# Optimization experiments

Measured on AMD Instinct MI355X. Metric: run time of the kernel, lower is better.

Reference implementation:

```python
import jax, jax.numpy as jnp
import numpy as np
from jax import lax

B, D, K = 65536, 256, 32  # batch, num_latent_dims, flow_depth


def setup_inputs() -> dict:
    key = jax.random.key(0)
    k1, k2, k3, k4, k5 = jax.random.split(key, 5)
    X = jax.random.normal(k1, (B, D), dtype=jnp.float32)
    h = jax.random.normal(k2, (B, D), dtype=jnp.float32)  # passed through, unused by planar math
    u = jax.random.normal(k3, (K, D), dtype=jnp.float32) * 0.1
    w = jax.random.normal(k4, (K, D), dtype=jnp.float32) * 0.1
    b = jax.random.normal(k5, (K,), dtype=jnp.float32) * 0.1
    return {"X": X, "h": h, "u": u, "w": w, "b": b}


def _planar_chain(z0, u, w, b):
    """Sequential planar normalizing flow: z_{k+1} = z_k + u_hat_k * tanh(w_k.z_k + b_k)."""

    def step(z, params):
        u_k, w_k, b_k = params  # (D,), (D,), scalar
        # enforce invertibility: u_hat so that w.u_hat >= -1
        wu = jnp.dot(w_k, u_k)
        u_hat = u_k + (jax.nn.softplus(wu) - 1.0 - wu) * w_k / jnp.dot(w_k, w_k)
        lin = z @ w_k + b_k              # (B,)
        t = jnp.tanh(lin)                # (B,)
        z_new = z + t[:, None] * u_hat[None, :]
        # psi = (1 - t^2) w ; log|det J| = log|1 + psi.u_hat|
        log_det = jnp.log(jnp.abs(1.0 + (1.0 - t * t) * jnp.dot(w_k, u_hat)) + 1e-8)
        return z_new, log_det

    z_final, log_dets = lax.scan(step, z0, (u, w, b))
    return z_final, log_dets  # (B, D), (K, B)


def reference(X, h, u, w, b):
    z = X.reshape(X.shape[0], X.shape[1])  # view(B, D, -1) then view(B, D) -> (B, D)
    z_final, log_det_jacobians = _planar_chain(z, u, w, b)
    return z_final, log_det_jacobians
```

## Files before the change

### kernel.cpp

```cpp
#include <hip/hip_runtime.h>


#define B_ 65536
#define D_ 256
#define ROWS 128
#define GRID (B_ / ROWS)

#define WS_WT 0
#define WS_UH 8192
#define WS_G  16384
#define WS_C  17408

#define SW(c) (4 * (((c) + ((c) >> 3)) & 7))

__global__ __launch_bounds__(256) void nf_gen(const float* __restrict__ u_in,
                                              const float* __restrict__ w_in,
                                              float* __restrict__ ws) {
  __shared__ float wTg[8192];
  __shared__ float ug[8192];
  __shared__ float wu_s[32], ww_s[32], coefs_s[32];
  const int t = threadIdx.x;
  {
    const int k = t & 31, d0 = (t >> 5) * 32;
    const float4* wp = (const float4*)(w_in + k * 256 + d0);
#pragma unroll
    for (int q = 0; q < 8; ++q) {
      float4 v = wp[q];
      wTg[(d0 + q * 4 + 0) * 32 + k] = v.x;
      wTg[(d0 + q * 4 + 1) * 32 + k] = v.y;
      wTg[(d0 + q * 4 + 2) * 32 + k] = v.z;
      wTg[(d0 + q * 4 + 3) * 32 + k] = v.w;
    }
#pragma unroll
    for (int q = 0; q < 8; ++q)
      ((float4*)ug)[t + 256 * q] = ((const float4*)u_in)[t + 256 * q];
  }
  __syncthreads();
  const int k = t & 31, jg = t >> 5;
  float m1[4] = {0.f, 0.f, 0.f, 0.f}, m2[4] = {0.f, 0.f, 0.f, 0.f};
#pragma unroll 4
  for (int dc = 0; dc < 64; ++dc) {
    float wk[4];
    float4 wj[4], uj[4];
#pragma unroll
    for (int i = 0; i < 4; ++i) wk[i] = wTg[(dc * 4 + i) * 32 + k];
#pragma unroll
    for (int i = 0; i < 4; ++i) wj[i] = *(const float4*)&wTg[(dc * 4 + i) * 32 + jg * 4];
#pragma unroll
    for (int i = 0; i < 4; ++i) uj[i] = *(const float4*)&ug[(jg * 4 + i) * 256 + dc * 4];
#pragma unroll
    for (int i = 0; i < 4; ++i) {
      m1[i] = fmaf(uj[i].x, wk[0], m1[i]);
      m1[i] = fmaf(uj[i].y, wk[1], m1[i]);
      m1[i] = fmaf(uj[i].z, wk[2], m1[i]);
      m1[i] = fmaf(uj[i].w, wk[3], m1[i]);
    }
    const float* w0 = (const float*)&wj[0];
    const float* w1 = (const float*)&wj[1];
    const float* w2 = (const float*)&wj[2];
    const float* w3 = (const float*)&wj[3];
#pragma unroll
    for (int i = 0; i < 4; ++i) {
      m2[i] = fmaf(w0[i], wk[0], m2[i]);
      m2[i] = fmaf(w1[i], wk[1], m2[i]);
      m2[i] = fmaf(w2[i], wk[2], m2[i]);
      m2[i] = fmaf(w3[i], wk[3], m2[i]);
    }
  }
  if ((k >> 2) == jg) {
    wu_s[k] = m1[k & 3];
    ww_s[k] = m2[k & 3];
  }
  __syncthreads();
  if (t < 32) {
    float wu = wu_s[t], ww = ww_s[t];
    float sp = fmaxf(wu, 0.f) + log1pf(__expf(-fabsf(wu)));
    coefs_s[t] = (sp - 1.f - wu) / ww;
    ws[WS_C + t] = sp - 1.f;
  }
  __syncthreads();
#pragma unroll
  for (int i = 0; i < 4; ++i)
    ws[WS_G + k * 32 + jg * 4 + i] = fmaf(coefs_s[jg * 4 + i], m2[i], m1[i]);
  {
    const int k2 = t >> 3, d0 = (t & 7) * 32;
    const float ck = coefs_s[k2];
    const float4* up = (const float4*)(u_in + k2 * 256 + d0);
    const float4* wp2 = (const float4*)(w_in + k2 * 256 + d0);
    float4* od = (float4*)(ws + WS_UH + k2 * 256 + d0);
#pragma unroll
    for (int q = 0; q < 8; ++q) {
      float4 uv = up[q], wv = wp2[q];
      uv.x = fmaf(ck, wv.x, uv.x);
      uv.y = fmaf(ck, wv.y, uv.y);
      uv.z = fmaf(ck, wv.z, uv.z);
      uv.w = fmaf(ck, wv.w, uv.w);
      od[q] = uv;
    }
  }
#pragma unroll
  for (int q = 0; q < 8; ++q)
    ((float4*)(ws + WS_WT))[t + 256 * q] = ((const float4*)wTg)[t + 256 * q];
}

__global__ __launch_bounds__(256) void nf_fused(const float* __restrict__ X,
                                                const float* __restrict__ b_in,
                                                const float* __restrict__ ws,
                                                float* __restrict__ out) {
  __shared__ float wT[8192];
  __shared__ float us[8192];
  __shared__ float Xs[4096];
  const int t = threadIdx.x;
  const int row0 = blockIdx.x * ROWS;
  const int xoff = (t >> 6) * 32 + ((t >> 3) & 7) * 4;
  const int kq4 = (t & 7) * 4;
  const int row_ld = t >> 3;
  const int cl = t & 7;

#pragma unroll
  for (int q = 0; q < 8; ++q)
    ((float4*)wT)[t + 256 * q] = ((const float4*)(ws + WS_WT))[t + 256 * q];
#pragma unroll
  for (int q = 0; q < 8; ++q)
    ((float4*)us)[t + 256 * q] = ((const float4*)(ws + WS_UH))[t + 256 * q];

  float4 pf[4];
  auto load_stage = [&](int s) {
#pragma unroll
    for (int p = 0; p < 4; ++p)
      pf[p] = *(const float4*)(X + (size_t)(row0 + p * 32 + row_ld) * 256 + s * 32 + cl * 4);
  };
  auto store_stage = [&]() {
#pragma unroll
    for (int p = 0; p < 4; ++p) {
      const float f[4] = {pf[p].x, pf[p].y, pf[p].z, pf[p].w};
#pragma unroll
      for (int i = 0; i < 4; ++i) {
        const int c = cl * 4 + i;
        Xs[c * 128 + ((p * 32 + row_ld + SW(c)) & 127)] = f[i];
      }
    }
  };

  load_stage(0);
  __syncthreads();

  float p[4][4];
#pragma unroll
  for (int a = 0; a < 4; ++a)
#pragma unroll
    for (int b = 0; b < 4; ++b) p[a][b] = 0.f;

  for (int s = 0; s < 8; ++s) {
    store_stage();
    __syncthreads();
    if (s < 7) load_stage(s + 1);
#pragma unroll 8
    for (int dl = 0; dl < 32; ++dl) {
      float4 xv = *(const float4*)&Xs[dl * 128 + ((xoff + SW(dl)) & 127)];
      float4 wv = *(const float4*)&wT[(s * 32 + dl) * 32 + kq4];
      const float xr[4] = {xv.x, xv.y, xv.z, xv.w};
      const float wk[4] = {wv.x, wv.y, wv.z, wv.w};
#pragma unroll
      for (int a = 0; a < 4; ++a)
#pragma unroll
        for (int b = 0; b < 4; ++b) p[a][b] = fmaf(xr[a], wk[b], p[a][b]);
    }
    __syncthreads();
  }

#pragma unroll
  for (int b = 0; b < 4; ++b)
    *(float4*)&wT[(kq4 + b) * 128 + xoff] = make_float4(p[0][b], p[1][b], p[2][b], p[3][b]);
#pragma unroll
  for (int i = 0; i < 4; ++i) {
    const int e = t * 4 + i;
    Xs[(e >> 5) * 33 + (e & 31)] = ws[WS_G + e];
  }
  if (t < 32) {
    Xs[1536 + t] = ws[WS_C + t];
    Xs[1568 + t] = b_in[t];
  }
  __syncthreads();

  if (t < 128) {
    float pfull[32];
#pragma unroll
    for (int j = 0; j < 32; ++j) pfull[j] = wT[j * 128 + t] + Xs[1568 + j];
    float tvv[32];
#pragma unroll
    for (int kk = 0; kk < 32; ++kk) {
      float la = pfull[kk], lb = 0.f;
      const float* gp = &Xs[kk * 33];
#pragma unroll
      for (int j = 0; j + 1 < kk; j += 2) {
        la = fmaf(tvv[j], gp[j], la);
        lb = fmaf(tvv[j + 1], gp[j + 1], lb);
      }
      if (kk & 1) la = fmaf(tvv[kk - 1], gp[kk - 1], la);
      float lin = la + lb;
      float e = __expf(2.f * lin);
      float tk = 1.f - 2.f / (e + 1.f);
      tvv[kk] = tk;
      wT[4096 + kk * 128 + t] = tk;
      float val = fabsf(fmaf(1.f - tk * tk, Xs[1536 + kk], 1.f)) + 1e-8f;
      out[(size_t)B_ * D_ + (size_t)kk * B_ + row0 + t] = __logf(val);
    }
  }
  __syncthreads();

  const int cq8 = (t & 7) * 8;
  for (int cb = 0; cb < 4; ++cb) {
    const int c0 = cb * 64 + cq8;
    float acc[4][8];
#pragma unroll
    for (int a = 0; a < 4; ++a) {
      const float4 x0 = *(const float4*)(X + (size_t)(row0 + xoff + a) * 256 + c0);
      const float4 x1 = *(const float4*)(X + (size_t)(row0 + xoff + a) * 256 + c0 + 4);
      acc[a][0] = x0.x; acc[a][1] = x0.y; acc[a][2] = x0.z; acc[a][3] = x0.w;
      acc[a][4] = x1.x; acc[a][5] = x1.y; acc[a][6] = x1.z; acc[a][7] = x1.w;
    }
#pragma unroll 8
    for (int kk = 0; kk < 32; ++kk) {
      float4 t4 = *(const float4*)&wT[4096 + kk * 128 + xoff];
      float4 u0 = *(const float4*)&us[kk * 256 + c0];
      float4 u1 = *(const float4*)&us[kk * 256 + c0 + 4];
      const float tr[4] = {t4.x, t4.y, t4.z, t4.w};
      const float uk[8] = {u0.x, u0.y, u0.z, u0.w, u1.x, u1.y, u1.z, u1.w};
#pragma unroll
      for (int a = 0; a < 4; ++a)
#pragma unroll
        for (int b = 0; b < 8; ++b) acc[a][b] = fmaf(tr[a], uk[b], acc[a][b]);
    }
#pragma unroll
    for (int a = 0; a < 4; ++a) {
      float4* op = (float4*)(out + (size_t)(row0 + xoff + a) * 256 + c0);
      op[0] = make_float4(acc[a][0], acc[a][1], acc[a][2], acc[a][3]);
      op[1] = make_float4(acc[a][4], acc[a][5], acc[a][6], acc[a][7]);
    }
  }
}

extern "C" void kernel_launch(void* const* d_in, const int* in_sizes, int n_in,
                              void* d_out, int out_size, void* d_ws, size_t ws_size,
                              hipStream_t stream) {
  const float* X = (const float*)d_in[0];
  const float* u = (const float*)d_in[2];
  const float* w = (const float*)d_in[3];
  const float* b = (const float*)d_in[4];
  float* out = (float*)d_out;
  float* ws = (float*)d_ws;

  nf_gen<<<1, 256, 0, stream>>>(u, w, ws);
  nf_fused<<<GRID, 256, 0, stream>>>(X, b, ws, out);
}
```

Baseline: 204.5 us.

## Drop LDS staging of X, w and u_hat; read them directly from global memory

```diff
diff --git a/kernel.cpp b/kernel.cpp
--- a/kernel.cpp
+++ b/kernel.cpp
@@ -11,7 +11,12 @@
 #define WS_G  16384
 #define WS_C  17408
 
-#define SW(c) (4 * (((c) + ((c) >> 3)) & 7))
+#define P_STR 132
+#define T_OFF 4224
+#define G_OFF 8448
+#define C_OFF 9504
+#define BB_OFF 9536
+#define LDS_FLOATS 9568
 
 __global__ __launch_bounds__(256) void nf_gen(const float* __restrict__ u_in,
                                               const float* __restrict__ w_in,
@@ -107,91 +112,68 @@
                                                 const float* __restrict__ b_in,
                                                 const float* __restrict__ ws,
                                                 float* __restrict__ out) {
-  __shared__ float wT[8192];
-  __shared__ float us[8192];
-  __shared__ float Xs[4096];
+  __shared__ float lds[LDS_FLOATS];
+
   const int t = threadIdx.x;
   const int row0 = blockIdx.x * ROWS;
   const int xoff = (t >> 6) * 32 + ((t >> 3) & 7) * 4;
   const int kq4 = (t & 7) * 4;
-  const int row_ld = t >> 3;
-  const int cl = t & 7;
-
-#pragma unroll
-  for (int q = 0; q < 8; ++q)
-    ((float4*)wT)[t + 256 * q] = ((const float4*)(ws + WS_WT))[t + 256 * q];
-#pragma unroll
-  for (int q = 0; q < 8; ++q)
-    ((float4*)us)[t + 256 * q] = ((const float4*)(ws + WS_UH))[t + 256 * q];
-
-  float4 pf[4];
-  auto load_stage = [&](int s) {
-#pragma unroll
-    for (int p = 0; p < 4; ++p)
-      pf[p] = *(const float4*)(X + (size_t)(row0 + p * 32 + row_ld) * 256 + s * 32 + cl * 4);
-  };
-  auto store_stage = [&]() {
-#pragma unroll
-    for (int p = 0; p < 4; ++p) {
-      const float f[4] = {pf[p].x, pf[p].y, pf[p].z, pf[p].w};
-#pragma unroll
-      for (int i = 0; i < 4; ++i) {
-        const int c = cl * 4 + i;
-        Xs[c * 128 + ((p * 32 + row_ld + SW(c)) & 127)] = f[i];
+  const int cq8 = (t & 7) * 8;
+
+  float p[4][4];
+#pragma unroll
+  for (int a = 0; a < 4; ++a)
+#pragma unroll
+    for (int b2 = 0; b2 < 4; ++b2) p[a][b2] = 0.f;
+  {
+    const float* wbase = ws + WS_WT + kq4;
+    const float* xb = X + (size_t)(row0 + xoff) * 256;
+#pragma unroll 2
+    for (int dq = 0; dq < 64; ++dq) {
+      float4 wr[4];
+#pragma unroll
+      for (int i = 0; i < 4; ++i) wr[i] = *(const float4*)(wbase + (dq * 4 + i) * 32);
+      float4 xr[4];
+#pragma unroll
+      for (int a = 0; a < 4; ++a) xr[a] = *(const float4*)(xb + a * 256 + dq * 4);
+#pragma unroll
+      for (int a = 0; a < 4; ++a) {
+        const float xf[4] = {xr[a].x, xr[a].y, xr[a].z, xr[a].w};
+#pragma unroll
+        for (int i = 0; i < 4; ++i) {
+          p[a][0] = fmaf(xf[i], wr[i].x, p[a][0]);
+          p[a][1] = fmaf(xf[i], wr[i].y, p[a][1]);
+          p[a][2] = fmaf(xf[i], wr[i].z, p[a][2]);
+          p[a][3] = fmaf(xf[i], wr[i].w, p[a][3]);
+        }
       }
     }
-  };
-
-  load_stage(0);
-  __syncthreads();
-
-  float p[4][4];
-#pragma unroll
-  for (int a = 0; a < 4; ++a)
-#pragma unroll
-    for (int b = 0; b < 4; ++b) p[a][b] = 0.f;
-
-  for (int s = 0; s < 8; ++s) {
-    store_stage();
-    __syncthreads();
-    if (s < 7) load_stage(s + 1);
-#pragma unroll 8
-    for (int dl = 0; dl < 32; ++dl) {
-      float4 xv = *(const float4*)&Xs[dl * 128 + ((xoff + SW(dl)) & 127)];
-      float4 wv = *(const float4*)&wT[(s * 32 + dl) * 32 + kq4];
-      const float xr[4] = {xv.x, xv.y, xv.z, xv.w};
-      const float wk[4] = {wv.x, wv.y, wv.z, wv.w};
-#pragma unroll
-      for (int a = 0; a < 4; ++a)
-#pragma unroll
-        for (int b = 0; b < 4; ++b) p[a][b] = fmaf(xr[a], wk[b], p[a][b]);
-    }
-    __syncthreads();
-  }
-
-#pragma unroll
-  for (int b = 0; b < 4; ++b)
-    *(float4*)&wT[(kq4 + b) * 128 + xoff] = make_float4(p[0][b], p[1][b], p[2][b], p[3][b]);
+  }
+
+#pragma unroll
+  for (int b2 = 0; b2 < 4; ++b2)
+    *(float4*)&lds[(kq4 + b2) * P_STR + xoff] =
+        make_float4(p[0][b2], p[1][b2], p[2][b2], p[3][b2]);
 #pragma unroll
   for (int i = 0; i < 4; ++i) {
     const int e = t * 4 + i;
-    Xs[(e >> 5) * 33 + (e & 31)] = ws[WS_G + e];
+    lds[G_OFF + (e >> 5) * 33 + (e & 31)] = ws[WS_G + e];
   }
   if (t < 32) {
-    Xs[1536 + t] = ws[WS_C + t];
-    Xs[1568 + t] = b_in[t];
+    lds[C_OFF + t] = ws[WS_C + t];
+    lds[BB_OFF + t] = b_in[t];
   }
   __syncthreads();
 
   if (t < 128) {
     float pfull[32];
 #pragma unroll
-    for (int j = 0; j < 32; ++j) pfull[j] = wT[j * 128 + t] + Xs[1568 + j];
+    for (int j = 0; j < 32; ++j) pfull[j] = lds[j * P_STR + t] + lds[BB_OFF + j];
     float tvv[32];
 #pragma unroll
     for (int kk = 0; kk < 32; ++kk) {
       float la = pfull[kk], lb = 0.f;
-      const float* gp = &Xs[kk * 33];
+      const float* gp = &lds[G_OFF + kk * 33];
 #pragma unroll
       for (int j = 0; j + 1 < kk; j += 2) {
         la = fmaf(tvv[j], gp[j], la);
@@ -202,16 +184,15 @@
       float e = __expf(2.f * lin);
       float tk = 1.f - 2.f / (e + 1.f);
       tvv[kk] = tk;
-      wT[4096 + kk * 128 + t] = tk;
-      float val = fabsf(fmaf(1.f - tk * tk, Xs[1536 + kk], 1.f)) + 1e-8f;
+      lds[T_OFF + kk * P_STR + t] = tk;
+      float val = fabsf(fmaf(1.f - tk * tk, lds[C_OFF + kk], 1.f)) + 1e-8f;
       out[(size_t)B_ * D_ + (size_t)kk * B_ + row0 + t] = __logf(val);
     }
   }
   __syncthreads();
 
-  const int cq8 = (t & 7) * 8;
-  for (int cb = 0; cb < 4; ++cb) {
-    const int c0 = cb * 64 + cq8;
+  for (int cbk = 0; cbk < 4; ++cbk) {
+    const int c0 = cbk * 64 + cq8;
     float acc[4][8];
 #pragma unroll
     for (int a = 0; a < 4; ++a) {
@@ -220,17 +201,17 @@
       acc[a][0] = x0.x; acc[a][1] = x0.y; acc[a][2] = x0.z; acc[a][3] = x0.w;
       acc[a][4] = x1.x; acc[a][5] = x1.y; acc[a][6] = x1.z; acc[a][7] = x1.w;
     }
-#pragma unroll 8
+#pragma unroll 4
     for (int kk = 0; kk < 32; ++kk) {
-      float4 t4 = *(const float4*)&wT[4096 + kk * 128 + xoff];
-      float4 u0 = *(const float4*)&us[kk * 256 + c0];
-      float4 u1 = *(const float4*)&us[kk * 256 + c0 + 4];
+      float4 t4 = *(const float4*)&lds[T_OFF + kk * P_STR + xoff];
+      float4 u0 = *(const float4*)(ws + WS_UH + kk * 256 + c0);
+      float4 u1 = *(const float4*)(ws + WS_UH + kk * 256 + c0 + 4);
       const float tr[4] = {t4.x, t4.y, t4.z, t4.w};
       const float uk[8] = {u0.x, u0.y, u0.z, u0.w, u1.x, u1.y, u1.z, u1.w};
 #pragma unroll
       for (int a = 0; a < 4; ++a)
 #pragma unroll
-        for (int b = 0; b < 8; ++b) acc[a][b] = fmaf(tr[a], uk[b], acc[a][b]);
+        for (int b2 = 0; b2 < 8; ++b2) acc[a][b2] = fmaf(tr[a], uk[b2], acc[a][b2]);
     }
 #pragma unroll
     for (int a = 0; a < 4; ++a) {
```

New measurement: 223.8 us. 1.09x slower.

## Use bf16x3 split MFMA for projection and rank-K update GEMMs

Applied to the files above, without the earlier changes.

```diff
diff --git a/kernel.cpp b/kernel.cpp
--- a/kernel.cpp
+++ b/kernel.cpp
@@ -1,17 +1,39 @@
 #include <hip/hip_runtime.h>
 
+
+typedef __attribute__((ext_vector_type(8))) short short8;
+typedef __attribute__((ext_vector_type(4))) float f32x4;
 
 #define B_ 65536
 #define D_ 256
 #define ROWS 128
 #define GRID (B_ / ROWS)
 
-#define WS_WT 0
-#define WS_UH 8192
-#define WS_G  16384
-#define WS_C  17408
-
-#define SW(c) (4 * (((c) + ((c) >> 3)) & 7))
+#define WSB_WH 0
+#define WSB_WL 16896
+#define WSB_UTH 33792
+#define WSB_UTL 54272
+#define WSB_G 74752
+#define WSB_C 78848
+
+#define OFF_P 8448
+#define OFF_G 17696
+#define OFF_C 18752
+#define OFF_B 18784
+#define LDSF 18816
+#define WH_H 0
+#define WL_H 8448
+#define UH_H 0
+#define UL_H 10240
+#define XH_H 25152
+#define XL_H 30272
+
+__device__ __forceinline__ void bfsplit(float x, unsigned short& h, unsigned short& l) {
+  unsigned xb = __float_as_uint(x) & 0xffff0000u;
+  h = (unsigned short)(xb >> 16);
+  float r = x - __uint_as_float(xb);
+  l = (unsigned short)(__float_as_uint(r) >> 16);
+}
 
 __global__ __launch_bounds__(256) void nf_gen(const float* __restrict__ u_in,
                                               const float* __restrict__ w_in,
@@ -76,167 +98,219 @@
     float wu = wu_s[t], ww = ww_s[t];
     float sp = fmaxf(wu, 0.f) + log1pf(__expf(-fabsf(wu)));
     coefs_s[t] = (sp - 1.f - wu) / ww;
-    ws[WS_C + t] = sp - 1.f;
-  }
-  __syncthreads();
-#pragma unroll
-  for (int i = 0; i < 4; ++i)
-    ws[WS_G + k * 32 + jg * 4 + i] = fmaf(coefs_s[jg * 4 + i], m2[i], m1[i]);
+    ((float*)((char*)ws + WSB_C))[t] = sp - 1.f;
+  }
+  __syncthreads();
+  {
+    float* gws = (float*)((char*)ws + WSB_G);
+#pragma unroll
+    for (int i = 0; i < 4; ++i)
+      gws[k * 32 + jg * 4 + i] = fmaf(coefs_s[jg * 4 + i], m2[i], m1[i]);
+  }
   {
     const int k2 = t >> 3, d0 = (t & 7) * 32;
     const float ck = coefs_s[k2];
-    const float4* up = (const float4*)(u_in + k2 * 256 + d0);
+    unsigned short* whp = (unsigned short*)((char*)ws + WSB_WH);
+    unsigned short* wlp = (unsigned short*)((char*)ws + WSB_WL);
+    unsigned short* uthp = (unsigned short*)((char*)ws + WSB_UTH);
+    unsigned short* utlp = (unsigned short*)((char*)ws + WSB_UTL);
     const float4* wp2 = (const float4*)(w_in + k2 * 256 + d0);
-    float4* od = (float4*)(ws + WS_UH + k2 * 256 + d0);
+    const float4* up2 = (const float4*)(u_in + k2 * 256 + d0);
 #pragma unroll
     for (int q = 0; q < 8; ++q) {
-      float4 uv = up[q], wv = wp2[q];
-      uv.x = fmaf(ck, wv.x, uv.x);
-      uv.y = fmaf(ck, wv.y, uv.y);
-      uv.z = fmaf(ck, wv.z, uv.z);
-      uv.w = fmaf(ck, wv.w, uv.w);
-      od[q] = uv;
-    }
-  }
-#pragma unroll
-  for (int q = 0; q < 8; ++q)
-    ((float4*)(ws + WS_WT))[t + 256 * q] = ((const float4*)wTg)[t + 256 * q];
+      float4 wv = wp2[q], uv = up2[q];
+      const float wf[4] = {wv.x, wv.y, wv.z, wv.w};
+      const float uf[4] = {uv.x, uv.y, uv.z, uv.w};
+#pragma unroll
+      for (int i = 0; i < 4; ++i) {
+        unsigned short hh, ll;
+        bfsplit(wf[i], hh, ll);
+        whp[k2 * 264 + d0 + q * 4 + i] = hh;
+        wlp[k2 * 264 + d0 + q * 4 + i] = ll;
+        float uhv = fmaf(ck, wf[i], uf[i]);
+        bfsplit(uhv, hh, ll);
+        uthp[(d0 + q * 4 + i) * 40 + k2] = hh;
+        utlp[(d0 + q * 4 + i) * 40 + k2] = ll;
+      }
+    }
+  }
 }
 
 __global__ __launch_bounds__(256) void nf_fused(const float* __restrict__ X,
                                                 const float* __restrict__ b_in,
                                                 const float* __restrict__ ws,
                                                 float* __restrict__ out) {
-  __shared__ float wT[8192];
-  __shared__ float us[8192];
-  __shared__ float Xs[4096];
+  __shared__ __align__(16) float lds[LDSF];
+  unsigned short* ldsH = (unsigned short*)lds;
+
   const int t = threadIdx.x;
+  const int lane = t & 63;
+  const int wv = t >> 6;
+  const int ln15 = lane & 15;
+  const int g = lane >> 4;
+  const int g8 = g * 8, g4 = g * 4;
   const int row0 = blockIdx.x * ROWS;
-  const int xoff = (t >> 6) * 32 + ((t >> 3) & 7) * 4;
-  const int kq4 = (t & 7) * 4;
-  const int row_ld = t >> 3;
-  const int cl = t & 7;
-
-#pragma unroll
-  for (int q = 0; q < 8; ++q)
-    ((float4*)wT)[t + 256 * q] = ((const float4*)(ws + WS_WT))[t + 256 * q];
-#pragma unroll
-  for (int q = 0; q < 8; ++q)
-    ((float4*)us)[t + 256 * q] = ((const float4*)(ws + WS_UH))[t + 256 * q];
-
-  float4 pf[4];
-  auto load_stage = [&](int s) {
-#pragma unroll
-    for (int p = 0; p < 4; ++p)
-      pf[p] = *(const float4*)(X + (size_t)(row0 + p * 32 + row_ld) * 256 + s * 32 + cl * 4);
+
+  {
+    const uint4* wsrc = (const uint4*)((const char*)ws + WSB_WH);
+    uint4* wdst = (uint4*)lds;
+#pragma unroll
+    for (int i = 0; i < 8; ++i) wdst[t + 256 * i] = wsrc[t + 256 * i];
+    if (t < 64) wdst[2048 + t] = wsrc[2048 + t];
+  }
+#pragma unroll
+  for (int i = 0; i < 4; ++i) {
+    const int e = t * 4 + i;
+    lds[OFF_G + (e >> 5) * 33 + (e & 31)] = ((const float*)((const char*)ws + WSB_G))[e];
+  }
+  if (t < 32) {
+    lds[OFF_C + t] = ((const float*)((const char*)ws + WSB_C))[t];
+    lds[OFF_B + t] = b_in[t];
+  }
+
+  const int srow = t >> 1;
+  const int sdh = (t & 1) * 16;
+  float4 xr[4];
+  auto load_stage = [&](int cc) {
+    const float4* src = (const float4*)(X + (size_t)(row0 + srow) * 256 + cc * 32 + sdh);
+#pragma unroll
+    for (int j = 0; j < 4; ++j) xr[j] = src[j];
   };
   auto store_stage = [&]() {
-#pragma unroll
-    for (int p = 0; p < 4; ++p) {
-      const float f[4] = {pf[p].x, pf[p].y, pf[p].z, pf[p].w};
-#pragma unroll
-      for (int i = 0; i < 4; ++i) {
-        const int c = cl * 4 + i;
-        Xs[c * 128 + ((p * 32 + row_ld + SW(c)) & 127)] = f[i];
-      }
-    }
+    float xf[16];
+#pragma unroll
+    for (int j = 0; j < 4; ++j) {
+      xf[j * 4 + 0] = xr[j].x; xf[j * 4 + 1] = xr[j].y;
+      xf[j * 4 + 2] = xr[j].z; xf[j * 4 + 3] = xr[j].w;
+    }
+    short8 h0, h1, l0, l1;
+#pragma unroll
+    for (int e = 0; e < 8; ++e) {
+      unsigned short hh, ll;
+      bfsplit(xf[e], hh, ll);
+      h0[e] = (short)hh; l0[e] = (short)ll;
+      bfsplit(xf[8 + e], hh, ll);
+      h1[e] = (short)hh; l1[e] = (short)ll;
+    }
+    *(short8*)&ldsH[XH_H + srow * 40 + sdh] = h0;
+    *(short8*)&ldsH[XH_H + srow * 40 + sdh + 8] = h1;
+    *(short8*)&ldsH[XL_H + srow * 40 + sdh] = l0;
+    *(short8*)&ldsH[XL_H + srow * 40 + sdh + 8] = l1;
   };
 
+  f32x4 acc[2][2];
+#pragma unroll
+  for (int m = 0; m < 2; ++m)
+#pragma unroll
+    for (int n = 0; n < 2; ++n) acc[m][n] = (f32x4){0.f, 0.f, 0.f, 0.f};
+
   load_stage(0);
-  __syncthreads();
-
-  float p[4][4];
-#pragma unroll
-  for (int a = 0; a < 4; ++a)
-#pragma unroll
-    for (int b = 0; b < 4; ++b) p[a][b] = 0.f;
-
-  for (int s = 0; s < 8; ++s) {
+  for (int cc = 0; cc < 8; ++cc) {
     store_stage();
     __syncthreads();
-    if (s < 7) load_stage(s + 1);
-#pragma unroll 8
-    for (int dl = 0; dl < 32; ++dl) {
-      float4 xv = *(const float4*)&Xs[dl * 128 + ((xoff + SW(dl)) & 127)];
-      float4 wv = *(const float4*)&wT[(s * 32 + dl) * 32 + kq4];
-      const float xr[4] = {xv.x, xv.y, xv.z, xv.w};
-      const float wk[4] = {wv.x, wv.y, wv.z, wv.w};
-#pragma unroll
-      for (int a = 0; a < 4; ++a)
-#pragma unroll
-        for (int b = 0; b < 4; ++b) p[a][b] = fmaf(xr[a], wk[b], p[a][b]);
-    }
+    if (cc < 7) load_stage(cc + 1);
+    short8 ah[2], al[2], bh[2], bl[2];
+#pragma unroll
+    for (int m = 0; m < 2; ++m) {
+      const int hidx = XH_H + ((wv * 2 + m) * 16 + ln15) * 40 + g8;
+      ah[m] = *(const short8*)&ldsH[hidx];
+      al[m] = *(const short8*)&ldsH[hidx + (XL_H - XH_H)];
+    }
+#pragma unroll
+    for (int n = 0; n < 2; ++n) {
+      const int widx = (n * 16 + ln15) * 264 + cc * 32 + g8;
+      bh[n] = *(const short8*)&ldsH[WH_H + widx];
+      bl[n] = *(const short8*)&ldsH[WL_H + widx];
+    }
+#pragma unroll
+    for (int m = 0; m < 2; ++m)
+#pragma unroll
+      for (int n = 0; n < 2; ++n) {
+        acc[m][n] = __builtin_amdgcn_mfma_f32_16x16x32_bf16(ah[m], bh[n], acc[m][n], 0, 0, 0);
+        acc[m][n] = __builtin_amdgcn_mfma_f32_16x16x32_bf16(ah[m], bl[n], acc[m][n], 0, 0, 0);
+        acc[m][n] = __builtin_amdgcn_mfma_f32_16x16x32_bf16(al[m], bh[n], acc[m][n], 0, 0, 0);
+      }
     __syncthreads();
   }
 
 #pragma unroll
-  for (int b = 0; b < 4; ++b)
-    *(float4*)&wT[(kq4 + b) * 128 + xoff] = make_float4(p[0][b], p[1][b], p[2][b], p[3][b]);
-#pragma unroll
-  for (int i = 0; i < 4; ++i) {
-    const int e = t * 4 + i;
-    Xs[(e >> 5) * 33 + (e & 31)] = ws[WS_G + e];
-  }
-  if (t < 32) {
-    Xs[1536 + t] = ws[WS_C + t];
-    Xs[1568 + t] = b_in[t];
-  }
+  for (int m = 0; m < 2; ++m)
+#pragma unroll
+    for (int n = 0; n < 2; ++n)
+#pragma unroll
+      for (int q = 0; q < 4; ++q)
+        lds[OFF_P + (n * 16 + ln15) * 129 + ((wv * 2 + m) * 16 + g4 + q)] = acc[m][n][q];
   __syncthreads();
 
   if (t < 128) {
     float pfull[32];
 #pragma unroll
-    for (int j = 0; j < 32; ++j) pfull[j] = wT[j * 128 + t] + Xs[1568 + j];
+    for (int j = 0; j < 32; ++j) pfull[j] = lds[OFF_P + j * 129 + t] + lds[OFF_B + j];
     float tvv[32];
 #pragma unroll
     for (int kk = 0; kk < 32; ++kk) {
-      float la = pfull[kk], lb = 0.f;
-      const float* gp = &Xs[kk * 33];
+      float la = pfull[kk], lb2 = 0.f;
+      const float* gp = &lds[OFF_G + kk * 33];
 #pragma unroll
       for (int j = 0; j + 1 < kk; j += 2) {
         la = fmaf(tvv[j], gp[j], la);
-        lb = fmaf(tvv[j + 1], gp[j + 1], lb);
+        lb2 = fmaf(tvv[j + 1], gp[j + 1], lb2);
       }
       if (kk & 1) la = fmaf(tvv[kk - 1], gp[kk - 1], la);
-      float lin = la + lb;
+      float lin = la + lb2;
       float e = __expf(2.f * lin);
       float tk = 1.f - 2.f / (e + 1.f);
       tvv[kk] = tk;
-      wT[4096 + kk * 128 + t] = tk;
-      float val = fabsf(fmaf(1.f - tk * tk, Xs[1536 + kk], 1.f)) + 1e-8f;
+      float val = fabsf(fmaf(1.f - tk * tk, lds[OFF_C + kk], 1.f)) + 1e-8f;
       out[(size_t)B_ * D_ + (size_t)kk * B_ + row0 + t] = __logf(val);
     }
-  }
-  __syncthreads();
-
-  const int cq8 = (t & 7) * 8;
-  for (int cb = 0; cb < 4; ++cb) {
-    const int c0 = cb * 64 + cq8;
-    float acc[4][8];
-#pragma unroll
-    for (int a = 0; a < 4; ++a) {
-      const float4 x0 = *(const float4*)(X + (size_t)(row0 + xoff + a) * 256 + c0);
-      const float4 x1 = *(const float4*)(X + (size_t)(row0 + xoff + a) * 256 + c0 + 4);
-      acc[a][0] = x0.x; acc[a][1] = x0.y; acc[a][2] = x0.z; acc[a][3] = x0.w;
-      acc[a][4] = x1.x; acc[a][5] = x1.y; acc[a][6] = x1.z; acc[a][7] = x1.w;
-    }
-#pragma unroll 8
-    for (int kk = 0; kk < 32; ++kk) {
-      float4 t4 = *(const float4*)&wT[4096 + kk * 128 + xoff];
-      float4 u0 = *(const float4*)&us[kk * 256 + c0];
-      float4 u1 = *(const float4*)&us[kk * 256 + c0 + 4];
-      const float tr[4] = {t4.x, t4.y, t4.z, t4.w};
-      const float uk[8] = {u0.x, u0.y, u0.z, u0.w, u1.x, u1.y, u1.z, u1.w};
-#pragma unroll
-      for (int a = 0; a < 4; ++a)
-#pragma unroll
-        for (int b = 0; b < 8; ++b) acc[a][b] = fmaf(tr[a], uk[b], acc[a][b]);
-    }
-#pragma unroll
-    for (int a = 0; a < 4; ++a) {
-      float4* op = (float4*)(out + (size_t)(row0 + xoff + a) * 256 + c0);
-      op[0] = make_float4(acc[a][0], acc[a][1], acc[a][2], acc[a][3]);
-      op[1] = make_float4(acc[a][4], acc[a][5], acc[a][6], acc[a][7]);
+#pragma unroll
+    for (int q = 0; q < 4; ++q) {
+      short8 th, tl;
+#pragma unroll
+      for (int i = 0; i < 8; ++i) {
+        unsigned short hh, ll;
+        bfsplit(tvv[q * 8 + i], hh, ll);
+        th[i] = (short)hh;
+        tl[i] = (short)ll;
+      }
+      *(short8*)&ldsH[XH_H + t * 40 + q * 8] = th;
+      *(short8*)&ldsH[XL_H + t * 40 + q * 8] = tl;
+    }
+  }
+  __syncthreads();
+
+  {
+    const uint4* usrc = (const uint4*)((const char*)ws + WSB_UTH);
+    uint4* udst = (uint4*)lds;
+#pragma unroll
+    for (int i = 0; i < 10; ++i) udst[t + 256 * i] = usrc[t + 256 * i];
+  }
+  __syncthreads();
+
+  short8 tah[2], tal[2];
+#pragma unroll
+  for (int m = 0; m < 2; ++m) {
+    const int hidx = XH_H + ((wv * 2 + m) * 16 + ln15) * 40 + g8;
+    tah[m] = *(const short8*)&ldsH[hidx];
+    tal[m] = *(const short8*)&ldsH[hidx + (XL_H - XH_H)];
+  }
+  for (int Nt = 0; Nt < 16; ++Nt) {
+    const int uidx = (Nt * 16 + ln15) * 40 + g8;
+    short8 bh = *(const short8*)&ldsH[UH_H + uidx];
+    short8 bl = *(const short8*)&ldsH[UL_H + uidx];
+    const int col = Nt * 16 + ln15;
+#pragma unroll
+    for (int m = 0; m < 2; ++m) {
+      const size_t rbase = (size_t)row0 + (wv * 2 + m) * 16 + g4;
+      f32x4 c;
+#pragma unroll
+      for (int q = 0; q < 4; ++q) c[q] = X[(rbase + q) * 256 + col];
+      c = __builtin_amdgcn_mfma_f32_16x16x32_bf16(tah[m], bh, c, 0, 0, 0);
+      c = __builtin_amdgcn_mfma_f32_16x16x32_bf16(tah[m], bl, c, 0, 0, 0);
+      c = __builtin_amdgcn_mfma_f32_16x16x32_bf16(tal[m], bh, c, 0, 0, 0);
+#pragma unroll
+      for (int q = 0; q < 4; ++q) out[(rbase + q) * 256 + col] = c[q];
     }
   }
 }
```

Result: slower. 211.3 us (+3.4%).
